# Optimization experiments

Hardware: AMD Instinct MI355X
Metric: run time of the kernel (lower is better)

Reference implementation:

```python
import jax, jax.numpy as jnp
import numpy as np
import math

PERCENT = 0.5

def setup_inputs() -> dict:
    key = jax.random.key(0)
    x = jax.random.normal(key, (32, 128, 112, 112), dtype=jnp.float32)
    return {"x": x}

def reference(x):
    # x: [B, C, H, W]; per-pixel top-k over channels, keep values >= k-th largest, clamp at 0
    C = x.shape[1]
    k = math.ceil(PERCENT * C)
    xt = jnp.moveaxis(x, 1, -1)                 # [B, H, W, C]
    top_vals, _ = jax.lax.top_k(xt, k)          # [B, H, W, k]
    threshold = top_vals[..., -1:]              # k-th largest per pixel
    out = jnp.where(xt >= threshold, xt, jnp.float32(0.0))
    out = jnp.maximum(out, jnp.float32(0.0))    # clamp(min=0)
    return jnp.moveaxis(out, -1, 1)             # back to [B, C, H, W]
```

## Files before the change

kernel.cpp:

```cpp
#include <hip/hip_runtime.h>


#define CC        128
#define HWSZ      12544
#define PBLK      128
#define NBLK_PER_N 98

using f32x4 = __attribute__((ext_vector_type(4))) float;

__device__ __forceinline__ void bitonic64(float v[64]) {
  #pragma unroll
  for (int k = 2; k <= 64; k <<= 1) {
    #pragma unroll
    for (int j = k >> 1; j > 0; j >>= 1) {
      #pragma unroll
      for (int i = 0; i < 64; ++i) {
        int l = i ^ j;
        if (l > i) {
          float lo = fminf(v[i], v[l]);
          float hi = fmaxf(v[i], v[l]);
          bool up = ((i & k) == 0);
          v[i] = up ? lo : hi;
          v[l] = up ? hi : lo;
        }
      }
    }
  }
}

__global__ __launch_bounds__(256) void crelu_pct_kernel(
    const float* __restrict__ x, float* __restrict__ out) {
  __shared__ __align__(16) float thr_lds[PBLK];

  const int tid = threadIdx.x;
  const int n   = blockIdx.x / NBLK_PER_N;
  const int pb  = (blockIdx.x - n * NBLK_PER_N) * PBLK;

  const int ql   = tid >> 1;
  const int half = tid & 1;
  const size_t planeN = (size_t)CC * HWSZ;
  const float* xp = x + (size_t)n * planeN
                      + (size_t)(half << 6) * HWSZ
                      + (size_t)(pb + ql);

  float v[64];
  #pragma unroll
  for (int c = 0; c < 64; ++c) v[c] = xp[(size_t)c * HWSZ];
  bitonic64(v);

  float thr;
  {
    float mine  = half ? v[63] : v[0];
    float other = __shfl_xor(mine, 1, 64);
    thr = fmaxf(mine, other);
    #pragma unroll
    for (int i = 1; i < 64; ++i) {
      float m = half ? v[63 - i] : v[i];
      float o = __shfl_xor(m, 1, 64);
      thr = fminf(thr, fmaxf(m, o));
    }
  }
  if (!half) thr_lds[ql] = thr;
  __syncthreads();

  const int j  = tid & 31;
  const int c0 = tid >> 5;
  const f32x4 t4 = *reinterpret_cast<const f32x4*>(&thr_lds[j << 2]);
  const size_t rowpix = (size_t)n * planeN + (size_t)pb + (size_t)(j << 2);

  f32x4 w[16];
  #pragma unroll
  for (int i = 0; i < 16; ++i) {
    const int c = (i << 3) + c0;
    w[i] = *reinterpret_cast<const f32x4*>(x + rowpix + (size_t)c * HWSZ);
  }
  #pragma unroll
  for (int i = 0; i < 16; ++i) {
    const int c = (i << 3) + c0;
    f32x4 r;
    #pragma unroll
    for (int e = 0; e < 4; ++e)
      r[e] = (w[i][e] >= t4[e] && w[i][e] > 0.0f) ? w[i][e] : 0.0f;
    __builtin_nontemporal_store(
        r, reinterpret_cast<f32x4*>(out + rowpix + (size_t)c * HWSZ));
  }
}

extern "C" void kernel_launch(void* const* d_in, const int* in_sizes, int n_in,
                              void* d_out, int out_size, void* d_ws, size_t ws_size,
                              hipStream_t stream) {
  const float* x = (const float*)d_in[0];
  float* out = (float*)d_out;
  const int npix = in_sizes[0] / CC;
  const int grid = npix / PBLK;
  crelu_pct_kernel<<<grid, 256, 0, stream>>>(x, out);
}
```

Baseline: 354.4 us.

## Split per-pixel top-k across four lanes with bitonic merge via shuffles

Each pixel's 128 channels are now handled by four threads that each sort 32 values, then merge across lanes with xor-shuffles instead of two threads sorting 64 each. This cuts per-thread sort work and register pressure, so launch bounds can request 8 blocks per CU. Blocks cover 64 pixels instead of 128, and the second-pass loads of x are issued before the barrier so they overlap the threshold exchange. The cost is more shuffle traffic and twice as many smaller blocks.

Result: no change. 357.9 us (+1.0%).

```diff
diff --git a/kernel.cpp b/kernel.cpp
--- a/kernel.cpp
+++ b/kernel.cpp
@@ -3,18 +3,18 @@
 
 #define CC        128
 #define HWSZ      12544
-#define PBLK      128
-#define NBLK_PER_N 98
+#define PBLK      64
+#define NBLK_PER_N 196
 
 using f32x4 = __attribute__((ext_vector_type(4))) float;
 
-__device__ __forceinline__ void bitonic64(float v[64]) {
+__device__ __forceinline__ void sort32(float v[32]) {
   #pragma unroll
-  for (int k = 2; k <= 64; k <<= 1) {
+  for (int k = 2; k <= 32; k <<= 1) {
     #pragma unroll
     for (int j = k >> 1; j > 0; j >>= 1) {
       #pragma unroll
-      for (int i = 0; i < 64; ++i) {
+      for (int i = 0; i < 32; ++i) {
         int l = i ^ j;
         if (l > i) {
           float lo = fminf(v[i], v[l]);
@@ -28,55 +28,89 @@
   }
 }
 
-__global__ __launch_bounds__(256) void crelu_pct_kernel(
+__device__ __forceinline__ void clean32(float v[32]) {
+  #pragma unroll
+  for (int j = 16; j > 0; j >>= 1) {
+    #pragma unroll
+    for (int i = 0; i < 32; ++i) {
+      int l = i ^ j;
+      if (l > i) {
+        float lo = fminf(v[i], v[l]);
+        float hi = fmaxf(v[i], v[l]);
+        v[i] = lo;
+        v[l] = hi;
+      }
+    }
+  }
+}
+
+__global__ __launch_bounds__(256, 8) void crelu_pct_kernel(
     const float* __restrict__ x, float* __restrict__ out) {
   __shared__ __align__(16) float thr_lds[PBLK];
 
   const int tid = threadIdx.x;
   const int n   = blockIdx.x / NBLK_PER_N;
   const int pb  = (blockIdx.x - n * NBLK_PER_N) * PBLK;
+  const size_t planeN = (size_t)CC * HWSZ;
 
-  const int ql   = tid >> 1;
-  const int half = tid & 1;
-  const size_t planeN = (size_t)CC * HWSZ;
+  const int q   = tid >> 2;
+  const int grp = tid & 3;
   const float* xp = x + (size_t)n * planeN
-                      + (size_t)(half << 6) * HWSZ
-                      + (size_t)(pb + ql);
+                      + (size_t)(grp << 5) * HWSZ
+                      + (size_t)(pb + q);
 
-  float v[64];
+  float v[32];
   #pragma unroll
-  for (int c = 0; c < 64; ++c) v[c] = xp[(size_t)c * HWSZ];
-  bitonic64(v);
+  for (int c = 0; c < 32; ++c) v[c] = xp[(size_t)c * HWSZ];
+  sort32(v);
 
-  float thr;
   {
-    float mine  = half ? v[63] : v[0];
-    float other = __shfl_xor(mine, 1, 64);
-    thr = fmaxf(mine, other);
+    const bool upper = (grp & 1);
     #pragma unroll
-    for (int i = 1; i < 64; ++i) {
-      float m = half ? v[63 - i] : v[i];
-      float o = __shfl_xor(m, 1, 64);
-      thr = fminf(thr, fmaxf(m, o));
+    for (int i = 0; i < 16; ++i) {
+      const int ir = 31 - i;
+      float oa = __shfl_xor(v[ir], 1, 64);
+      float ob = __shfl_xor(v[i],  1, 64);
+      float loa = fminf(v[i],  oa), hia = fmaxf(v[i],  oa);
+      float lob = fminf(v[ir], ob), hib = fmaxf(v[ir], ob);
+      v[i]  = upper ? hia : loa;
+      v[ir] = upper ? hib : lob;
     }
+    clean32(v);
   }
-  if (!half) thr_lds[ql] = thr;
-  __syncthreads();
 
-  const int j  = tid & 31;
-  const int c0 = tid >> 5;
-  const f32x4 t4 = *reinterpret_cast<const f32x4*>(&thr_lds[j << 2]);
+  float thr = 3.4e38f;
+  {
+    #pragma unroll
+    for (int i = 0; i < 16; ++i) {
+      const int ir = 31 - i;
+      float oa = __shfl_xor(v[ir], 3, 64);
+      float ob = __shfl_xor(v[i],  3, 64);
+      thr = fminf(thr, fmaxf(v[i],  oa));
+      thr = fminf(thr, fmaxf(v[ir], ob));
+    }
+    thr = fminf(thr, __shfl_xor(thr, 1, 64));
+    thr = fminf(thr, __shfl_xor(thr, 2, 64));
+  }
+  if (grp == 0) thr_lds[q] = thr;
+
+  const int j  = tid & 15;
+  const int c0 = tid >> 4;
   const size_t rowpix = (size_t)n * planeN + (size_t)pb + (size_t)(j << 2);
 
-  f32x4 w[16];
+  f32x4 w[8];
   #pragma unroll
-  for (int i = 0; i < 16; ++i) {
-    const int c = (i << 3) + c0;
+  for (int i = 0; i < 8; ++i) {
+    const int c = (i << 4) + c0;
     w[i] = *reinterpret_cast<const f32x4*>(x + rowpix + (size_t)c * HWSZ);
   }
+
+  __syncthreads();
+  const f32x4 t4 = *reinterpret_cast<const f32x4*>(&thr_lds[j << 2]);
+
   #pragma unroll
-  for (int i = 0; i < 16; ++i) {
-    const int c = (i << 3) + c0;
+  for (int i = 0; i < 8; ++i) {
+    const int c = (i << 4) + c0;
     f32x4 r;
     #pragma unroll
     for (int e = 0; e < 4; ++e)
```
